# Kernel tuning notes

Measured on AMD Instinct MI355X. Metric: run time of the kernel, lower is better.

Reference implementation:

```python
import jax, jax.numpy as jnp
import numpy as np
from jax import lax

B, T, D, H, W = 2, 16, 64, 64, 64
E, HID, K = 4, 128, 3
NS = 0.01  # noise_scale
EPS = 1e-5  # LayerNorm eps (torch default)


def setup_inputs() -> dict:
    key = jax.random.key(0)
    ks = jax.random.split(key, 20)
    r = lambda i, shape, s=1.0: jax.random.normal(ks[i], shape, dtype=jnp.float32) * s
    return {
        "x_real": r(0, (B, T, D, H, W)),
        "x_imag": r(1, (B, T, D, H, W)),
        "dt": jax.random.uniform(ks[2], (B, T), dtype=jnp.float32, minval=0.1, maxval=1.0),
        "noise_eps_real": r(3, (B * H * W, T, D)),
        "noise_eps_imag": r(4, (B * H * W, T, D)),
        "ln_s_w": jnp.ones((2 * D,), jnp.float32),
        "ln_s_b": jnp.zeros((2 * D,), jnp.float32),
        "conv_w": r(5, (K, K, 2 * D, 2 * D), 0.02),  # HWIO
        "conv_b": jnp.zeros((2 * D,), jnp.float32),
        "ln_t_w": jnp.ones((2 * D,), jnp.float32),
        "ln_t_b": jnp.zeros((2 * D,), jnp.float32),
        "lam_re": r(6, (D,)),
        "lam_im": r(7, (D,)),
        "src_bias_re": r(8, (D,), 0.02),
        "src_bias_im": r(9, (D,), 0.02),
        "enc_re": r(10, (D, D), 0.125),
        "enc_im": r(11, (D, D), 0.125),
        "dec_re": r(12, (D, D), 0.125),
        "dec_im": r(13, (D, D), 0.125),
        "router_w": r(14, (2 * D, E), 0.02),
        "router_b": jnp.zeros((E,), jnp.float32),
        "w1": r(15, (E, 2 * D, HID), 0.02),
        "b1": jnp.zeros((E, HID), jnp.float32),
        "w2": r(16, (E, HID, 2 * D), 0.02),
        "b2": jnp.zeros((E, 2 * D), jnp.float32),
    }


def _complex_ln(zr, zi, w, b):
    # LayerNorm over concatenated [real, imag] last dim, then re-split to complex
    zc = jnp.concatenate([zr, zi], axis=-1)
    mu = jnp.mean(zc, -1, keepdims=True)
    var = jnp.var(zc, -1, keepdims=True)
    zn = (zc - mu) * lax.rsqrt(var + EPS) * w + b
    r, i = jnp.split(zn, 2, axis=-1)
    return r + 1j * i


def reference(x_real, x_imag, dt, noise_eps_real, noise_eps_imag,
              ln_s_w, ln_s_b, conv_w, conv_b, ln_t_w, ln_t_b,
              lam_re, lam_im, src_bias_re, src_bias_im,
              enc_re, enc_im, dec_re, dec_im,
              router_w, router_b, w1, b1, w2, b2):
    x = x_real + 1j * x_imag  # (B,T,D,H,W) complex
    resid = x
    # --- spatial: complex norm + clifford-style conv on stacked real/imag channels ---
    xs = jnp.transpose(x.reshape(B * T, D, H, W), (0, 2, 3, 1))  # (BT,H,W,D)
    zn = _complex_ln(xs.real, xs.imag, ln_s_w, ln_s_b)
    xc = jnp.concatenate([zn.real, zn.imag], axis=-1)  # (BT,H,W,2D)
    y = lax.conv_general_dilated(xc, conv_w, (1, 1), 'SAME',
                                 dimension_numbers=('NHWC', 'HWIO', 'NHWC')) + conv_b
    yr, yi = jnp.split(y, 2, axis=-1)
    x = jnp.transpose(yr + 1j * yi, (0, 3, 1, 2)).reshape(B, T, D, H, W) + resid
    resid = x
    # --- temporal: eigen-basis encode, decay-forced parallel scan, decode ---
    xt = jnp.transpose(x, (0, 3, 4, 1, 2)).reshape(B * H * W, T, D)
    xt = _complex_ln(xt.real, xt.imag, ln_t_w, ln_t_b)  # complex (N,T,D)
    dtE = jnp.broadcast_to(dt[:, None, None, :], (B, H, W, T)).reshape(B * H * W, T)
    lam = -jax.nn.softplus(lam_re) + 1j * lam_im  # stable per-mode eigenvalues (D,)
    a = jnp.exp(lam[None, None, :] * dtE[:, :, None])  # decay op (N,T,D)
    forcing = (a - 1.0) / lam  # ZOH forcing op
    Eb = enc_re + 1j * enc_im
    bias = src_bias_re + 1j * src_bias_im
    u = (jnp.einsum('ntd,de->nte', xt, Eb) + bias) * forcing
    u = u + NS * jnp.sqrt(dtE)[:, :, None] * (noise_eps_real + 1j * noise_eps_imag)

    def comb(c1, c2):  # first-order linear recurrence h_t = a_t h_{t-1} + u_t
        a1, b1_ = c1
        a2, b2_ = c2
        return a1 * a2, b1_ * a2 + b2_

    _, h = lax.associative_scan(comb, (a, u), axis=1)
    Db = dec_re + 1j * dec_im
    drift = jnp.einsum('nte,ed->ntd', h, Db).real  # (N,T,D)
    x = jnp.transpose(drift.reshape(B, H, W, T, D), (0, 3, 4, 1, 2)) + resid
    # --- MoE FFN on per-pixel tokens (real/imag concat) ---
    tc = jnp.transpose(x, (0, 1, 3, 4, 2))  # (B,T,H,W,D) complex
    tok = jnp.concatenate([tc.real, tc.imag], axis=-1).reshape(-1, 2 * D)  # (N2,2D)
    gates = jax.nn.softmax(tok @ router_w + router_b, axis=-1)  # (N2,E)
    hdn = jax.nn.gelu(jnp.einsum('nd,edh->neh', tok, w1) + b1)
    yo = jnp.einsum('neh,eho->neo', hdn, w2) + b2
    out = jnp.einsum('ne,neo->no', gates, yo)
    dr, di = jnp.split(out, 2, axis=-1)
    delta = jnp.transpose((dr + 1j * di).reshape(B, T, H, W, D), (0, 1, 4, 2, 3))
    x = x + delta
    return jnp.stack([x.real, x.imag], axis=0)  # (2,B,T,D,H,W)
```

## Files before the change

kernel.cpp:

```cpp
#include <hip/hip_runtime.h>
#include <hip/hip_bf16.h>
#include <math.h>

#define HW 4096
#define TP 264

typedef __attribute__((ext_vector_type(8))) short bf16x8;
typedef _Float16 f16x8 __attribute__((ext_vector_type(8)));
typedef __attribute__((ext_vector_type(4))) float f32x4;

#define MFMA_BF16(a, b, c) __builtin_amdgcn_mfma_f32_16x16x32_bf16((a), (b), (c), 0, 0, 0)
#define MFMA_F16(a, b, c)  __builtin_amdgcn_mfma_f32_16x16x32_f16((a), (b), (c), 0, 0, 0)

static __device__ __forceinline__ float gelu_f(float xv) {
    float x2 = xv*xv;
    float t2 = xv*(1.5957691216057308f + 0.07135481627260025f*x2);
    float ee = __expf(t2);
    return xv*(1.f - __builtin_amdgcn_rcpf(ee + 1.f));
}

__global__ __launch_bounds__(256) void k_prep_t(
    const float* __restrict__ src, __hip_bfloat16* __restrict__ dst)
{
    __shared__ float t[32*33];
    int m  = blockIdx.x;
    int tr = blockIdx.y >> 2, tc = blockIdx.y & 3;
    int tid = threadIdx.x;
    for (int l = tid; l < 1024; l += 256) {
        int r = l >> 5, c = l & 31;
        t[r*33 + c] = src[m*16384 + (tr*32 + r)*128 + (tc*32 + c)];
    }
    __syncthreads();
    for (int l = tid; l < 1024; l += 256) {
        int c = l >> 5, r = l & 31;
        dst[m*16384 + (tc*32 + c)*128 + (tr*32 + r)] = __float2bfloat16(t[r*33 + c]);
    }
}

__global__ __launch_bounds__(256) void k_prep_enc(
    const float* __restrict__ encr, const float* __restrict__ enci,
    const float* __restrict__ decr, const float* __restrict__ deci,
    const float* __restrict__ dt,
    const float* __restrict__ lamr, const float* __restrict__ lami,
    const float* __restrict__ rw,
    _Float16* __restrict__ Benc, _Float16* __restrict__ BdecX,
    float4* __restrict__ coefG, float* __restrict__ nscG,
    __hip_bfloat16* __restrict__ rwB)
{
    int idx = blockIdx.x*256 + threadIdx.x;
    if (idx < 16384) {
        int n = idx >> 7, k = idx & 127;
        int e = n & 63, d = k & 63;
        float v;
        if (n < 64) v = (k < 64) ? encr[d*64 + e] : -enci[d*64 + e];
        else        v = (k < 64) ? enci[d*64 + e] :  encr[d*64 + e];
        Benc[idx] = (_Float16)v;
    }
    if (idx < 16384) {
        int n = idx >> 8, k = idx & 255;
        int kk = k & 127;
        int e = kk & 63;
        float v = (kk < 64) ? decr[e*64 + n] : -deci[e*64 + n];
        BdecX[idx] = (_Float16)v;
    }
    if (idx < 2048) {
        int bt = idx >> 6, e = idx & 63;
        float dtv = dt[bt];
        float lr = lamr[e];
        float sp = (lr > 20.f) ? lr : log1pf(expf(lr));
        float lre = -sp, lim = lami[e];
        float inv = 1.f / (lre*lre + lim*lim);
        float ex = expf(lre*dtv);
        float sn, cs; sincosf(lim*dtv, &sn, &cs);
        float ar = ex*cs, ai = ex*sn;
        float fr = ((ar - 1.f)*lre + ai*lim)*inv;
        float fi = (ai*lre - (ar - 1.f)*lim)*inv;
        coefG[idx] = make_float4(ar, ai, fr, fi);
    }
    if (idx < 2048) {
        int n = idx >> 7, k = idx & 127;
        float v = (n < 4) ? rw[k*4 + n] : 0.f;
        rwB[idx] = __float2bfloat16(v);
    }
    if (idx < 32) nscG[idx] = 0.01f * sqrtf(dt[idx]);
}

__global__ __launch_bounds__(256) void k_ln_s(
    const float* __restrict__ xr, const float* __restrict__ xi,
    const float* __restrict__ lw, const float* __restrict__ lb,
    __hip_bfloat16* __restrict__ out)
{
    __shared__ float tile[64*129];
    __shared__ float ps[64*4];
    __shared__ float ps2[64*4];
    __shared__ float mu_s[64];
    __shared__ float rs_s[64];
    int bt  = blockIdx.x;
    int hw0 = blockIdx.y * 64;
    int tid = threadIdx.x;
    int wl = tid & 63;
    int q  = tid >> 6;
    float s = 0.f, s2 = 0.f;
    for (int c = q; c < 128; c += 4) {
        const float* src = (c < 64) ? xr : xi;
        int d = c & 63;
        float v = src[(bt*64 + d)*HW + hw0 + wl];
        tile[wl*129 + c] = v;
        s += v; s2 += v*v;
    }
    ps[wl*4 + q] = s;
    ps2[wl*4 + q] = s2;
    __syncthreads();
    if (tid < 64) {
        float ss = ps[tid*4+0]+ps[tid*4+1]+ps[tid*4+2]+ps[tid*4+3];
        float qq = ps2[tid*4+0]+ps2[tid*4+1]+ps2[tid*4+2]+ps2[tid*4+3];
        float mu = ss * 0.0078125f;
        float var = qq * 0.0078125f - mu*mu;
        mu_s[tid] = mu;
        rs_s[tid] = rsqrtf(var + 1e-5f);
    }
    __syncthreads();
    int c = tid & 127;
    int r = tid >> 7;
    float wc = lw[c], bc = lb[c];
    for (int wi = r; wi < 64; wi += 2) {
        float v = tile[wi*129 + c];
        out[(size_t)(bt*HW + hw0 + wi)*128 + c] =
            __float2bfloat16((v - mu_s[wi]) * rs_s[wi] * wc + bc);
    }
}

__global__ __launch_bounds__(256) void k_conv_mfma(
    const __hip_bfloat16* __restrict__ xc,
    const __hip_bfloat16* __restrict__ wB,
    const float* __restrict__ cb,
    const float* __restrict__ xr, const float* __restrict__ xi,
    float* __restrict__ x1)
{
    __shared__ __align__(16) short inrow[3*66*136];
    int bt = blockIdx.x, h = blockIdx.y;
    int tid = threadIdx.x;
    if (tid < 96) {
        int r = tid / 32, t2 = tid & 31;
        int px = (t2 & 1) ? 65 : 0;
        int j = t2 >> 1;
        *(float4*)&inrow[(r*66 + px)*136 + j*8] = make_float4(0.f,0.f,0.f,0.f);
    }
    for (int c = tid; c < 3072; c += 256) {
        int r   = c >> 10;
        int rem = c & 1023;
        int px  = rem >> 4;
        int j   = rem & 15;
        int gh  = h + r - 1;
        float4 v = make_float4(0.f,0.f,0.f,0.f);
        if ((unsigned)gh < 64u)
            v = *(const float4*)&xc[(size_t)((bt*HW + gh*64 + px)*128) + j*8];
        *(float4*)&inrow[(r*66 + px + 1)*136 + j*8] = v;
    }
    __syncthreads();

    int wv = tid >> 6, l = tid & 63, lm = l & 15, q = l >> 4;
    int n0 = wv * 32;
    f32x4 acc[4][2];
    #pragma unroll
    for (int mi = 0; mi < 4; mi++)
        #pragma unroll
        for (int ni = 0; ni < 2; ni++)
            acc[mi][ni] = (f32x4){0.f,0.f,0.f,0.f};

    for (int p = 0; p < 9; p++) {
        int kh = p / 3, kw = p - kh*3;
        const __hip_bfloat16* wp = wB + p*16384;
        int abase = (kh*66 + kw)*136;
        #pragma unroll
        for (int ks = 0; ks < 4; ks++) {
            int ko = ks*32 + q*8;
            bf16x8 b0 = *(const bf16x8*)(wp + (n0 + lm)*128 + ko);
            bf16x8 b1 = *(const bf16x8*)(wp + (n0 + 16 + lm)*128 + ko);
            #pragma unroll
            for (int mi = 0; mi < 4; mi++) {
                bf16x8 a = *(const bf16x8*)&inrow[abase + (mi*16 + lm)*136 + ko];
                acc[mi][0] = MFMA_BF16(a, b0, acc[mi][0]);
                acc[mi][1] = MFMA_BF16(a, b1, acc[mi][1]);
            }
        }
    }
    #pragma unroll
    for (int ni = 0; ni < 2; ni++) {
        int oc = n0 + ni*16 + lm;
        float bias = cb[oc];
        const float* rsp = (oc < 64) ? xr : xi;
        const float* rbase = &rsp[(bt*64 + (oc & 63))*HW + h*64];
        #pragma unroll
        for (int mi = 0; mi < 4; mi++) {
            #pragma unroll
            for (int r = 0; r < 4; r++) {
                int w = mi*16 + q*4 + r;
                x1[(size_t)(bt*HW + h*64 + w)*128 + oc] = acc[mi][ni][r] + bias + rbase[w];
            }
        }
    }
}

__global__ __launch_bounds__(128) void k_temporal_mfma(
    float* xio,
    const float* __restrict__ lw, const float* __restrict__ lb,
    const float* __restrict__ sbr, const float* __restrict__ sbi,
    const _Float16* __restrict__ Benc, const _Float16* __restrict__ BdecX,
    const float4* __restrict__ coefG, const float* __restrict__ nscG,
    const float* __restrict__ nzr, const float* __restrict__ nzi)
{
    __shared__ __align__(16) short At[64*TP];
    int n0  = blockIdx.x * 4;
    int b   = n0 >> 12;
    int hw0 = n0 & 4095;
    int tid = threadIdx.x;

    {
        int row = tid >> 1, half = tid & 1;
        int nl = row >> 4, t = row & 15;
        const float4* src = (const float4*)&xio[((size_t)((b*16 + t)*HW) + hw0 + nl)*128 + half*64];
        float4 v[16];
        float s = 0.f, s2 = 0.f;
        #pragma unroll
        for (int j = 0; j < 16; j++) {
            v[j] = src[j];
            s  += v[j].x + v[j].y + v[j].z + v[j].w;
            s2 += v[j].x*v[j].x + v[j].y*v[j].y + v[j].z*v[j].z + v[j].w*v[j].w;
        }
        s  += __shfl_xor(s, 1, 64);
        s2 += __shfl_xor(s2, 1, 64);
        float mu  = s * 0.0078125f;
        float var = s2 * 0.0078125f - mu*mu;
        float rsq = rsqrtf(var + 1e-5f);
        const float4* lw4 = (const float4*)(lw + half*64);
        const float4* lb4 = (const float4*)(lb + half*64);
        short* dstrow = &At[row*TP + half*64];
        #pragma unroll
        for (int j = 0; j < 16; j++) {
            float4 wv4 = lw4[j], bv = lb4[j];
            union { _Float16 h[4]; float2 f; } u;
            u.h[0] = (_Float16)((v[j].x - mu)*rsq*wv4.x + bv.x);
            u.h[1] = (_Float16)((v[j].y - mu)*rsq*wv4.y + bv.y);
            u.h[2] = (_Float16)((v[j].z - mu)*rsq*wv4.z + bv.z);
            u.h[3] = (_Float16)((v[j].w - mu)*rsq*wv4.w + bv.w);
            *(float2*)(dstrow + j*4) = u.f;
        }
    }
    __syncthreads();

    int wv = tid >> 6, l = tid & 63, lm = l & 15, q = l >> 4;

    f32x4 acc[2][8];
    #pragma unroll
    for (int mi = 0; mi < 2; mi++)
        #pragma unroll
        for (int ni = 0; ni < 8; ni++)
            acc[mi][ni] = (f32x4){0.f,0.f,0.f,0.f};
    #pragma unroll
    for (int ks = 0; ks < 4; ks++) {
        int ko = ks*32 + q*8;
        f16x8 a0 = *(const f16x8*)&At[((2*wv+0)*16 + lm)*TP + ko];
        f16x8 a1 = *(const f16x8*)&At[((2*wv+1)*16 + lm)*TP + ko];
        #pragma unroll
        for (int ni = 0; ni < 8; ni++) {
            f16x8 bb = *(const f16x8*)(Benc + (ni*16 + lm)*128 + ko);
            acc[0][ni] = MFMA_F16(a0, bb, acc[0][ni]);
            acc[1][ni] = MFMA_F16(a1, bb, acc[1][ni]);
        }
    }

    int btbase = b*16;
    #pragma unroll
    for (int ni = 0; ni < 4; ni++) {
        int e = ni*16 + lm;
        float br = sbr[e], bi = sbi[e];
        float4 cf[4]; float ns[4];
        #pragma unroll
        for (int r = 0; r < 4; r++) {
            int t = q*4 + r;
            cf[r] = coefG[(btbase + t)*64 + e];
            ns[r] = nscG[btbase + t];
        }
        #pragma unroll
        for (int mi = 0; mi < 2; mi++) {
            int nl = 2*wv + mi;
            int ng = n0 + nl;
            float nrv[4], niv[4];
            #pragma unroll
            for (int r = 0; r < 4; r++) {
                int off = (ng*16 + q*4 + r)*64 + e;
                nrv[r] = nzr[off];
                niv[r] = nzi[off];
            }
            float hr = 0.f, hi = 0.f, Apr = 1.f, Api = 0.f;
            float hrs[4], his[4], Aprs[4], Apis[4];
            #pragma unroll
            for (int r = 0; r < 4; r++) {
                float Sr = acc[mi][ni][r] + br;
                float Si = acc[mi][ni+4][r] + bi;
                float ur = Sr*cf[r].z - Si*cf[r].w + ns[r]*nrv[r];
                float ui = Sr*cf[r].w + Si*cf[r].z + ns[r]*niv[r];
                if (r == 0) { hr = ur; hi = ui; Apr = cf[0].x; Api = cf[0].y; }
                else {
                    float tr = cf[r].x*hr - cf[r].y*hi + ur;
                    float ti = cf[r].x*hi + cf[r].y*hr + ui;
                    hr = tr; hi = ti;
                    tr = cf[r].x*Apr - cf[r].y*Api;
                    ti = cf[r].x*Api + cf[r].y*Apr;
                    Apr = tr; Api = ti;
                }
                hrs[r] = hr; his[r] = hi; Aprs[r] = Apr; Apis[r] = Api;
            }
            float Ar = Apr, Ai = Api, Hr = hr, Hi = hi;
            #pragma unroll
            for (int off = 16; off <= 32; off <<= 1) {
                float pAr = __shfl_up(Ar, off, 64);
                float pAi = __shfl_up(Ai, off, 64);
                float pHr = __shfl_up(Hr, off, 64);
                float pHi = __shfl_up(Hi, off, 64);
                if (l >= off) {
                    Hr = Hr + Ar*pHr - Ai*pHi;
                    Hi = Hi + Ar*pHi + Ai*pHr;
                    float tAr = Ar*pAr - Ai*pAi;
                    float tAi = Ar*pAi + Ai*pAr;
                    Ar = tAr; Ai = tAi;
                }
            }
            float gr = __shfl_up(Hr, 16, 64);
            float gi = __shfl_up(Hi, 16, 64);
            if (q == 0) { gr = 0.f; gi = 0.f; }
            #pragma unroll
            for (int r = 0; r < 4; r++) {
                float fhr = hrs[r] + Aprs[r]*gr - Apis[r]*gi;
                float fhi = his[r] + Aprs[r]*gi + Apis[r]*gr;
                int row = nl*16 + q*4 + r;
                _Float16 hrh = (_Float16)fhr;
                _Float16 hih = (_Float16)fhi;
                *(_Float16*)&At[row*TP + e]        = hrh;
                *(_Float16*)&At[row*TP + 64 + e]   = hih;
                *(_Float16*)&At[row*TP + 128 + e]  = (_Float16)(fhr - (float)hrh);
                *(_Float16*)&At[row*TP + 192 + e]  = (_Float16)(fhi - (float)hih);
            }
        }
    }

    f32x4 acc2[2][4];
    #pragma unroll
    for (int mi = 0; mi < 2; mi++)
        #pragma unroll
        for (int ni = 0; ni < 4; ni++)
            acc2[mi][ni] = (f32x4){0.f,0.f,0.f,0.f};
    #pragma unroll
    for (int ks = 0; ks < 8; ks++) {
        int ko = ks*32 + q*8;
        f16x8 a0 = *(const f16x8*)&At[((2*wv+0)*16 + lm)*TP + ko];
        f16x8 a1 = *(const f16x8*)&At[((2*wv+1)*16 + lm)*TP + ko];
        #pragma unroll
        for (int ni = 0; ni < 4; ni++) {
            f16x8 bb = *(const f16x8*)(BdecX + (ni*16 + lm)*256 + ko);
            acc2[0][ni] = MFMA_F16(a0, bb, acc2[0][ni]);
            acc2[1][ni] = MFMA_F16(a1, bb, acc2[1][ni]);
        }
    }

    #pragma unroll
    for (int mi = 0; mi < 2; mi++) {
        int nl = 2*wv + mi;
        #pragma unroll
        for (int ni = 0; ni < 4; ni++) {
            int d = ni*16 + lm;
            #pragma unroll
            for (int r = 0; r < 4; r++) {
                int t = q*4 + r;
                size_t idx = ((size_t)((b*16 + t)*HW) + hw0 + nl)*128 + d;
                xio[idx] = xio[idx] + acc2[mi][ni][r];
            }
        }
    }
}

__global__ __launch_bounds__(256) void k_moe_mfma(
    const float* __restrict__ xio,
    float* __restrict__ outp,
    const __hip_bfloat16* __restrict__ rwB, const float* __restrict__ rb,
    const __hip_bfloat16* __restrict__ w1b, const float* __restrict__ b1,
    const __hip_bfloat16* __restrict__ w2b, const float* __restrict__ b2)
{
    __shared__ __align__(16) short smem[2*64*136];
    __shared__ float gates[256];
    short* tokA = smem;
    short* hidA = smem + 64*136;
    float* tile = (float*)smem;
    int tok0 = blockIdx.x * 64;
    int tid = threadIdx.x;
    for (int lsd = tid; lsd < 2048; lsd += 256) {
        int t = lsd >> 5, j = lsd & 31;
        float4 v = *(const float4*)&xio[(size_t)(tok0 + t)*128 + j*4];
        union { __hip_bfloat16 h[4]; float2 f; } u;
        u.h[0] = __float2bfloat16(v.x);
        u.h[1] = __float2bfloat16(v.y);
        u.h[2] = __float2bfloat16(v.z);
        u.h[3] = __float2bfloat16(v.w);
        *(float2*)&tokA[t*136 + j*4] = u.f;
    }
    __syncthreads();

    int wv = tid >> 6, l = tid & 63, lm = l & 15, q = l >> 4;
    int n0 = wv * 32;

    {
        f32x4 racc[2];
        racc[0] = (f32x4){0.f,0.f,0.f,0.f};
        racc[1] = (f32x4){0.f,0.f,0.f,0.f};
        #pragma unroll
        for (int ks = 0; ks < 4; ks++) {
            int ko = ks*32 + q*8;
            bf16x8 bb = *(const bf16x8*)(rwB + lm*128 + ko);
            bf16x8 a0 = *(const bf16x8*)&tokA[(n0 + lm)*136 + ko];
            bf16x8 a1 = *(const bf16x8*)&tokA[(n0 + 16 + lm)*136 + ko];
            racc[0] = MFMA_BF16(a0, bb, racc[0]);
            racc[1] = MFMA_BF16(a1, bb, racc[1]);
        }
        float rb_l = rb[lm & 3];
        #pragma unroll
        for (int mi = 0; mi < 2; mi++) {
            #pragma unroll
            for (int r = 0; r < 4; r++) {
                float g = racc[mi][r] + rb_l;
                float mx = fmaxf(g, __shfl_xor(g, 1, 64));
                mx = fmaxf(mx, __shfl_xor(mx, 2, 64));
                float ev = __expf(g - mx);
                float sv = ev + __shfl_xor(ev, 1, 64);
                sv += __shfl_xor(sv, 2, 64);
                if (lm < 4)
                    gates[(n0 + mi*16 + q*4 + r)*4 + lm] = ev * __builtin_amdgcn_rcpf(sv);
            }
        }
    }

    f32x4 outa[4][2];
    #pragma unroll
    for (int mi = 0; mi < 4; mi++)
        #pragma unroll
        for (int ni = 0; ni < 2; ni++)
            outa[mi][ni] = (f32x4){0.f,0.f,0.f,0.f};

    for (int e = 0; e < 4; e++) {
        f32x4 acc1[4][2];
        #pragma unroll
        for (int mi = 0; mi < 4; mi++)
            #pragma unroll
            for (int ni = 0; ni < 2; ni++)
                acc1[mi][ni] = (f32x4){0.f,0.f,0.f,0.f};
        const __hip_bfloat16* wp1 = w1b + e*16384;
        #pragma unroll
        for (int ks = 0; ks < 4; ks++) {
            int ko = ks*32 + q*8;
            bf16x8 b0  = *(const bf16x8*)(wp1 + (n0 + lm)*128 + ko);
            bf16x8 b1v = *(const bf16x8*)(wp1 + (n0 + 16 + lm)*128 + ko);
            #pragma unroll
            for (int mi = 0; mi < 4; mi++) {
                bf16x8 a = *(const bf16x8*)&tokA[(mi*16 + lm)*136 + ko];
                acc1[mi][0] = MFMA_BF16(a, b0,  acc1[mi][0]);
                acc1[mi][1] = MFMA_BF16(a, b1v, acc1[mi][1]);
            }
        }
        #pragma unroll
        for (int ni = 0; ni < 2; ni++) {
            int hcol = n0 + ni*16 + lm;
            float bb = b1[e*128 + hcol];
            #pragma unroll
            for (int mi = 0; mi < 4; mi++) {
                #pragma unroll
                for (int r = 0; r < 4; r++) {
                    float hv = gelu_f(acc1[mi][ni][r] + bb);
                    int m = mi*16 + q*4 + r;
                    *(__hip_bfloat16*)&hidA[m*136 + hcol] = __float2bfloat16(hv);
                }
            }
        }
        __syncthreads();
        f32x4 acc2[4][2];
        #pragma unroll
        for (int mi = 0; mi < 4; mi++)
            #pragma unroll
            for (int ni = 0; ni < 2; ni++)
                acc2[mi][ni] = (f32x4){0.f,0.f,0.f,0.f};
        const __hip_bfloat16* wp2 = w2b + e*16384;
        #pragma unroll
        for (int ks = 0; ks < 4; ks++) {
            int ko = ks*32 + q*8;
            bf16x8 b0  = *(const bf16x8*)(wp2 + (n0 + lm)*128 + ko);
            bf16x8 b1v = *(const bf16x8*)(wp2 + (n0 + 16 + lm)*128 + ko);
            #pragma unroll
            for (int mi = 0; mi < 4; mi++) {
                bf16x8 a = *(const bf16x8*)&hidA[(mi*16 + lm)*136 + ko];
                acc2[mi][0] = MFMA_BF16(a, b0,  acc2[mi][0]);
                acc2[mi][1] = MFMA_BF16(a, b1v, acc2[mi][1]);
            }
        }
        #pragma unroll
        for (int ni = 0; ni < 2; ni++) {
            int ocol = n0 + ni*16 + lm;
            float bb = b2[e*128 + ocol];
            #pragma unroll
            for (int mi = 0; mi < 4; mi++) {
                #pragma unroll
                for (int r = 0; r < 4; r++) {
                    int m = mi*16 + q*4 + r;
                    float g = gates[m*4 + e];
                    outa[mi][ni][r] += g * (acc2[mi][ni][r] + bb);
                }
            }
        }
        __syncthreads();
    }

    #pragma unroll
    for (int ni = 0; ni < 2; ni++) {
        int col = n0 + ni*16 + lm;
        #pragma unroll
        for (int mi = 0; mi < 4; mi++) {
            #pragma unroll
            for (int r = 0; r < 4; r++) {
                int m = mi*16 + q*4 + r;
                tile[m*129 + col] = xio[(size_t)(tok0 + m)*128 + col] + outa[mi][ni][r];
            }
        }
    }
    __syncthreads();
    int bt = tok0 >> 12;
    int hw0 = tok0 & 4095;
    for (int lid = tid; lid < 8192; lid += 256) {
        int c = lid >> 6, m = lid & 63;
        int p = c >> 6, d = c & 63;
        outp[((size_t)((p*32 + bt)*64 + d))*HW + hw0 + m] = tile[m*129 + c];
    }
}

extern "C" void kernel_launch(void* const* d_in, const int* in_sizes, int n_in,
                              void* d_out, int out_size, void* d_ws, size_t ws_size,
                              hipStream_t stream)
{
    const float* x_real = (const float*)d_in[0];
    const float* x_imag = (const float*)d_in[1];
    const float* dt     = (const float*)d_in[2];
    const float* nzr    = (const float*)d_in[3];
    const float* nzi    = (const float*)d_in[4];
    const float* ln_s_w = (const float*)d_in[5];
    const float* ln_s_b = (const float*)d_in[6];
    const float* conv_w = (const float*)d_in[7];
    const float* conv_b = (const float*)d_in[8];
    const float* ln_t_w = (const float*)d_in[9];
    const float* ln_t_b = (const float*)d_in[10];
    const float* lam_re = (const float*)d_in[11];
    const float* lam_im = (const float*)d_in[12];
    const float* sbr    = (const float*)d_in[13];
    const float* sbi    = (const float*)d_in[14];
    const float* enc_re = (const float*)d_in[15];
    const float* enc_im = (const float*)d_in[16];
    const float* dec_re = (const float*)d_in[17];
    const float* dec_im = (const float*)d_in[18];
    const float* rw     = (const float*)d_in[19];
    const float* rb     = (const float*)d_in[20];
    const float* w1     = (const float*)d_in[21];
    const float* b1     = (const float*)d_in[22];
    const float* w2     = (const float*)d_in[23];
    const float* b2     = (const float*)d_in[24];

    char* ws = (char*)d_ws;
    float* bufA = (float*)ws;
    __hip_bfloat16* bufB = (__hip_bfloat16*)(ws + (size_t)64*1024*1024);
    __hip_bfloat16* wBc  = (__hip_bfloat16*)(ws + (size_t)96*1024*1024);
    __hip_bfloat16* w1b  = wBc + 9*16384;
    __hip_bfloat16* w2b  = w1b + 4*16384;
    _Float16* Benc  = (_Float16*)(w2b + 4*16384);
    _Float16* BdecX = Benc + 16384;
    float4* coefG = (float4*)(BdecX + 16384);
    float* nscG   = (float*)(coefG + 2048);
    __hip_bfloat16* rwB = (__hip_bfloat16*)(nscG + 32);
    float* outp = (float*)d_out;

    k_prep_t  <<<dim3(9,16), 256, 0, stream>>>(conv_w, wBc);
    k_prep_t  <<<dim3(4,16), 256, 0, stream>>>(w1, w1b);
    k_prep_t  <<<dim3(4,16), 256, 0, stream>>>(w2, w2b);
    k_prep_enc<<<64,         256, 0, stream>>>(enc_re, enc_im, dec_re, dec_im,
                                               dt, lam_re, lam_im, rw,
                                               Benc, BdecX, coefG, nscG, rwB);

    k_ln_s         <<<dim3(32,64), 256, 0, stream>>>(x_real, x_imag, ln_s_w, ln_s_b, bufB);
    k_conv_mfma    <<<dim3(32,64), 256, 0, stream>>>(bufB, wBc, conv_b, x_real, x_imag, bufA);
    k_temporal_mfma<<<2048,        128, 0, stream>>>(bufA, ln_t_w, ln_t_b, sbr, sbi,
                                                     Benc, BdecX, coefG, nscG, nzr, nzi);
    k_moe_mfma     <<<2048,        256, 0, stream>>>(bufA, outp, rwB, rb, w1b, b1, w2b, b2);
}
```

Baseline: 504.6 us.

## Fuse spatial LayerNorm into conv kernel, recomputing halo rows per block

Removes the separate spatial LayerNorm kernel and its bf16 intermediate buffer. The conv kernel now reads the fp32 input rows (the current row plus one neighbour on each side), computes per-pixel LayerNorm statistics, and writes normalized bf16 values straight into shared memory. This saves one kernel launch and a write and read of the intermediate through global memory. In exchange each input row is read and normalized three times (once per neighbouring block), and there are extra block-wide syncs and 32 values held in registers per thread.

```diff
diff --git a/kernel.cpp b/kernel.cpp
--- a/kernel.cpp
+++ b/kernel.cpp
@@ -85,81 +85,83 @@
     if (idx < 32) nscG[idx] = 0.01f * sqrtf(dt[idx]);
 }
 
-__global__ __launch_bounds__(256) void k_ln_s(
+__global__ __launch_bounds__(256) void k_conv_mfma(
     const float* __restrict__ xr, const float* __restrict__ xi,
     const float* __restrict__ lw, const float* __restrict__ lb,
-    __hip_bfloat16* __restrict__ out)
+    const __hip_bfloat16* __restrict__ wB,
+    const float* __restrict__ cb,
+    float* __restrict__ x1)
 {
-    __shared__ float tile[64*129];
+    __shared__ __align__(16) short inrow[3*66*136];
     __shared__ float ps[64*4];
     __shared__ float ps2[64*4];
     __shared__ float mu_s[64];
     __shared__ float rs_s[64];
-    int bt  = blockIdx.x;
-    int hw0 = blockIdx.y * 64;
+    __shared__ float lwS[128];
+    __shared__ float lbS[128];
+    int bt = blockIdx.x, h = blockIdx.y;
     int tid = threadIdx.x;
     int wl = tid & 63;
     int q  = tid >> 6;
-    float s = 0.f, s2 = 0.f;
-    for (int c = q; c < 128; c += 4) {
-        const float* src = (c < 64) ? xr : xi;
-        int d = c & 63;
-        float v = src[(bt*64 + d)*HW + hw0 + wl];
-        tile[wl*129 + c] = v;
-        s += v; s2 += v*v;
-    }
-    ps[wl*4 + q] = s;
-    ps2[wl*4 + q] = s2;
-    __syncthreads();
-    if (tid < 64) {
-        float ss = ps[tid*4+0]+ps[tid*4+1]+ps[tid*4+2]+ps[tid*4+3];
-        float qq = ps2[tid*4+0]+ps2[tid*4+1]+ps2[tid*4+2]+ps2[tid*4+3];
-        float mu = ss * 0.0078125f;
-        float var = qq * 0.0078125f - mu*mu;
-        mu_s[tid] = mu;
-        rs_s[tid] = rsqrtf(var + 1e-5f);
-    }
-    __syncthreads();
-    int c = tid & 127;
-    int r = tid >> 7;
-    float wc = lw[c], bc = lb[c];
-    for (int wi = r; wi < 64; wi += 2) {
-        float v = tile[wi*129 + c];
-        out[(size_t)(bt*HW + hw0 + wi)*128 + c] =
-            __float2bfloat16((v - mu_s[wi]) * rs_s[wi] * wc + bc);
-    }
-}
-
-__global__ __launch_bounds__(256) void k_conv_mfma(
-    const __hip_bfloat16* __restrict__ xc,
-    const __hip_bfloat16* __restrict__ wB,
-    const float* __restrict__ cb,
-    const float* __restrict__ xr, const float* __restrict__ xi,
-    float* __restrict__ x1)
-{
-    __shared__ __align__(16) short inrow[3*66*136];
-    int bt = blockIdx.x, h = blockIdx.y;
-    int tid = threadIdx.x;
-    if (tid < 96) {
-        int r = tid / 32, t2 = tid & 31;
+
+    if (tid < 128) { lwS[tid] = lw[tid]; lbS[tid] = lb[tid]; }
+    if (tid >= 128 && tid < 224) {
+        int t = tid - 128;
+        int r = t / 32, t2 = t & 31;
         int px = (t2 & 1) ? 65 : 0;
         int j = t2 >> 1;
         *(float4*)&inrow[(r*66 + px)*136 + j*8] = make_float4(0.f,0.f,0.f,0.f);
     }
-    for (int c = tid; c < 3072; c += 256) {
-        int r   = c >> 10;
-        int rem = c & 1023;
-        int px  = rem >> 4;
-        int j   = rem & 15;
-        int gh  = h + r - 1;
-        float4 v = make_float4(0.f,0.f,0.f,0.f);
-        if ((unsigned)gh < 64u)
-            v = *(const float4*)&xc[(size_t)((bt*HW + gh*64 + px)*128) + j*8];
-        *(float4*)&inrow[(r*66 + px + 1)*136 + j*8] = v;
+
+    const float* srcb = (q < 2) ? xr : xi;
+    int dbase = (q & 1) * 32;
+    for (int r = 0; r < 3; r++) {
+        int gh = h + r - 1;
+        bool ok = ((unsigned)gh < 64u);
+        float v[32];
+        if (ok) {
+            float s = 0.f, s2 = 0.f;
+            const float* base = &srcb[((size_t)(bt*64 + dbase))*HW + gh*64 + wl];
+            #pragma unroll
+            for (int k = 0; k < 32; k++) {
+                float vv = base[(size_t)k*HW];
+                v[k] = vv; s += vv; s2 += vv*vv;
+            }
+            ps [wl*4 + q] = s;
+            ps2[wl*4 + q] = s2;
+        }
+        __syncthreads();
+        if (ok && tid < 64) {
+            float ss = ps[tid*4+0]+ps[tid*4+1]+ps[tid*4+2]+ps[tid*4+3];
+            float qq = ps2[tid*4+0]+ps2[tid*4+1]+ps2[tid*4+2]+ps2[tid*4+3];
+            float mu = ss * 0.0078125f;
+            float var = qq * 0.0078125f - mu*mu;
+            mu_s[tid] = mu;
+            rs_s[tid] = rsqrtf(var + 1e-5f);
+        }
+        __syncthreads();
+        short* drow = &inrow[(r*66 + wl + 1)*136 + q*32];
+        if (ok) {
+            float mu = mu_s[wl], rs = rs_s[wl];
+            #pragma unroll
+            for (int j = 0; j < 4; j++) {
+                union { __hip_bfloat16 hh[8]; float4 f; } u;
+                #pragma unroll
+                for (int k = 0; k < 8; k++) {
+                    int c = q*32 + j*8 + k;
+                    u.hh[k] = __float2bfloat16((v[j*8+k] - mu)*rs*lwS[c] + lbS[c]);
+                }
+                *(float4*)&drow[j*8] = u.f;
+            }
+        } else {
+            float4 z = make_float4(0.f,0.f,0.f,0.f);
+            #pragma unroll
+            for (int j = 0; j < 4; j++) *(float4*)&drow[j*8] = z;
+        }
     }
     __syncthreads();
 
-    int wv = tid >> 6, l = tid & 63, lm = l & 15, q = l >> 4;
+    int wv = tid >> 6, l = tid & 63, lm = l & 15, qq2 = l >> 4;
     int n0 = wv * 32;
     f32x4 acc[4][2];
     #pragma unroll
@@ -174,7 +176,7 @@
         int abase = (kh*66 + kw)*136;
         #pragma unroll
         for (int ks = 0; ks < 4; ks++) {
-            int ko = ks*32 + q*8;
+            int ko = ks*32 + qq2*8;
             bf16x8 b0 = *(const bf16x8*)(wp + (n0 + lm)*128 + ko);
             bf16x8 b1 = *(const bf16x8*)(wp + (n0 + 16 + lm)*128 + ko);
             #pragma unroll
@@ -195,7 +197,7 @@
         for (int mi = 0; mi < 4; mi++) {
             #pragma unroll
             for (int r = 0; r < 4; r++) {
-                int w = mi*16 + q*4 + r;
+                int w = mi*16 + qq2*4 + r;
                 x1[(size_t)(bt*HW + h*64 + w)*128 + oc] = acc[mi][ni][r] + bias + rbase[w];
             }
         }
@@ -571,7 +573,6 @@
 
     char* ws = (char*)d_ws;
     float* bufA = (float*)ws;
-    __hip_bfloat16* bufB = (__hip_bfloat16*)(ws + (size_t)64*1024*1024);
     __hip_bfloat16* wBc  = (__hip_bfloat16*)(ws + (size_t)96*1024*1024);
     __hip_bfloat16* w1b  = wBc + 9*16384;
     __hip_bfloat16* w2b  = w1b + 4*16384;
@@ -589,8 +590,8 @@
                                                dt, lam_re, lam_im, rw,
                                                Benc, BdecX, coefG, nscG, rwB);
 
-    k_ln_s         <<<dim3(32,64), 256, 0, stream>>>(x_real, x_imag, ln_s_w, ln_s_b, bufB);
-    k_conv_mfma    <<<dim3(32,64), 256, 0, stream>>>(bufB, wBc, conv_b, x_real, x_imag, bufA);
+    k_conv_mfma    <<<dim3(32,64), 256, 0, stream>>>(x_real, x_imag, ln_s_w, ln_s_b,
+                                                     wBc, conv_b, bufA);
     k_temporal_mfma<<<2048,        128, 0, stream>>>(bufA, ln_t_w, ln_t_b, sbr, sbi,
                                                      Benc, BdecX, coefG, nscG, nzr, nzi);
     k_moe_mfma     <<<2048,        256, 0, stream>>>(bufA, outp, rwB, rb, w1b, b1, w2b, b2);
```

Measured after the change: 471.6 us. 6.5% less time.
